# Optimization experiments

Measured on AMD Instinct MI355X. Metric: run time of the kernel, lower is better.

Reference implementation:

```python
import jax, jax.numpy as jnp
import numpy as np

B, S, D, H, HD = 2, 4096, 1024, 16, 64   # batch, seq, hidden, heads, head_dim
BLOCK, W = 64, 8                          # block size, local window in blocks (512 tokens)
ROPE_BASE = 10000.0


def _rope_tables(seq_len, dim, dtype):
    inv_freq = 1.0 / (ROPE_BASE ** (jnp.arange(0, dim, 2, dtype=jnp.float32) / dim))
    t = jnp.arange(seq_len, dtype=jnp.float32)
    freqs = jnp.einsum('i,j->ij', t, inv_freq)          # [S, dim/2]
    emb = jnp.concatenate([freqs, freqs], axis=-1)       # [S, dim]
    return jnp.cos(emb).astype(dtype), jnp.sin(emb).astype(dtype)


def _rotate_half(x):
    x1, x2 = x[..., : x.shape[-1] // 2], x[..., x.shape[-1] // 2:]
    return jnp.concatenate([-x2, x1], axis=-1)


def _apply_rope(q, k, position_ids):
    # q, k: [B, H, S, HD]; position_ids: [B, S]
    cos_t, sin_t = _rope_tables(S, HD, q.dtype)
    cos = cos_t[position_ids][:, None, :, :]             # [B, 1, S, HD]
    sin = sin_t[position_ids][:, None, :, :]
    q_emb = q * cos + _rotate_half(q) * sin
    k_emb = k * cos + _rotate_half(k) * sin
    return q_emb, k_emb


def _block_sparse_attention(q, k, v):
    # Causal block-sparse (sliding window of W blocks), DeepSpeed-style layout.
    # q, k, v: [B, H, S, HD]
    nb = S // BLOCK
    scale = 1.0 / jnp.sqrt(jnp.asarray(HD, q.dtype))
    qb = q.reshape(B, H, nb, BLOCK, HD)
    kb = k.reshape(B, H, nb, BLOCK, HD)
    vb = v.reshape(B, H, nb, BLOCK, HD)
    # block-column indices attended by each block-row: i-W+1 .. i
    idx = jnp.arange(nb)[:, None] - jnp.arange(W - 1, -1, -1)[None, :]   # [nb, W]
    valid = idx >= 0
    idxc = jnp.clip(idx, 0, nb - 1)
    kg = kb[:, :, idxc]                                   # [B, H, nb, W, BLOCK, HD]
    vg = vb[:, :, idxc]
    scores = jnp.einsum('bhnqd,bhnwkd->bhnqwk', qb, kg) * scale  # [B,H,nb,BLOCK,W,BLOCK]
    # absolute positions for causal mask within the window
    qpos = (jnp.arange(nb) * BLOCK)[:, None, None, None] + jnp.arange(BLOCK)[None, :, None, None]  # [nb,BLOCK,1,1]
    kpos = (idxc * BLOCK)[:, None, :, None] + jnp.arange(BLOCK)[None, None, None, :]               # [nb,1,W,BLOCK]
    mask = (kpos <= qpos) & valid[:, None, :, None]       # [nb, BLOCK, W, BLOCK]
    neg = jnp.asarray(-1e9, scores.dtype)
    scores = jnp.where(mask[None, None], scores, neg)
    scores = scores.reshape(B, H, nb, BLOCK, W * BLOCK)
    probs = jax.nn.softmax(scores, axis=-1)
    out = jnp.einsum('bhnqk,bhnkd->bhnqd', probs, vg.reshape(B, H, nb, W * BLOCK, HD))
    return out.reshape(B, H, S, HD)


def setup_inputs() -> dict:
    key = jax.random.key(0)
    ks = jax.random.split(key, 5)
    hidden_states = jax.random.normal(ks[0], (B, S, D), dtype=jnp.float32)
    position_ids = jnp.tile(jnp.arange(S, dtype=jnp.int32)[None, :], (B, 1))
    w_init = lambda k: (jax.random.normal(k, (D, D), dtype=jnp.float32) * 0.02)
    return {
        'hidden_states': hidden_states,
        'position_ids': position_ids,
        'wq': w_init(ks[1]),  # stored [in, out]
        'wk': w_init(ks[2]),
        'wv': w_init(ks[3]),
        'wo': w_init(ks[4]),
    }


def reference(hidden_states, position_ids, wq, wk, wv, wo):
    q = jnp.einsum('bsd,de->bse', hidden_states, wq).reshape(B, S, H, HD).transpose(0, 2, 1, 3)
    k = jnp.einsum('bsd,de->bse', hidden_states, wk).reshape(B, S, H, HD).transpose(0, 2, 1, 3)
    v = jnp.einsum('bsd,de->bse', hidden_states, wv).reshape(B, S, H, HD).transpose(0, 2, 1, 3)
    q, k = _apply_rope(q, k, position_ids)
    attn = _block_sparse_attention(q, k, v)               # [B, H, S, HD]
    attn = attn.transpose(0, 2, 1, 3).reshape(B, S, D)
    return jnp.einsum('bsd,de->bse', attn, wo)
```

## Files before the change

kernel.cpp:

```cpp
#include <hip/hip_runtime.h>
#include <cstdint>
#include <cstddef>

#define B_ 2
#define S_ 4096
#define D_ 1024
#define H_ 16
#define HD_ 64
#define NB_ 64
#define W_ 8
#define M_ (B_*S_)

#define QSCALE 0.18033688011112042f
#define LOG2_10000_OVER_32 0.41524101186092034f

typedef __bf16 bf16_t;
typedef __bf16 bf16x8 __attribute__((ext_vector_type(8)));
typedef float f32x4 __attribute__((ext_vector_type(4)));

#define GLOAD_LDS16(gp, lp) \
  __builtin_amdgcn_global_load_lds((__attribute__((address_space(1))) void*)(gp), \
                                   (__attribute__((address_space(3))) void*)(lp), 16, 0, 0)
#define WAITV(n) asm volatile("s_waitcnt vmcnt(" #n ")" ::: "memory")
#define BAR() do { __builtin_amdgcn_s_barrier(); asm volatile("" ::: "memory"); } while (0)

__global__ __launch_bounds__(256) void prep_kernel(const float* __restrict__ hs,
                                                   bf16_t* __restrict__ hsb,
                                                   const float* __restrict__ w0,
                                                   const float* __restrict__ w1,
                                                   const float* __restrict__ w2,
                                                   const float* __restrict__ w3,
                                                   bf16_t* __restrict__ wT) {
  __shared__ float tile[32][33];
  const int bid = blockIdx.x;
  if (bid < (M_ * D_ / 4) / 256) {
    int i = bid * 256 + threadIdx.x;
    float4 v = ((const float4*)hs)[i];
    union { bf16_t b[4]; uint2 u; } cv;
    cv.b[0] = (bf16_t)v.x; cv.b[1] = (bf16_t)v.y; cv.b[2] = (bf16_t)v.z; cv.b[3] = (bf16_t)v.w;
    ((uint2*)hsb)[i] = cv.u;
  } else {
    const int b2 = bid - (M_ * D_ / 4) / 256;
    const int z = b2 >> 10;
    const int rem = b2 & 1023;
    const int bx = rem & 31, by = rem >> 5;
    const float* w = (z == 0) ? w0 : (z == 1) ? w1 : (z == 2) ? w2 : w3;
    bf16_t* wt = wT + (size_t)z * D_ * D_;
    const int tx = threadIdx.x & 31, ty = threadIdx.x >> 5;
    const int x = bx * 32 + tx;
    const int y0 = by * 32;
    for (int i = ty; i < 32; i += 8)
      tile[i][tx] = w[(size_t)(y0 + i) * D_ + x];
    __syncthreads();
    const int x2 = by * 32 + tx;
    const int y2 = bx * 32;
    for (int i = ty; i < 32; i += 8)
      wt[(size_t)(y2 + i) * D_ + x2] = (bf16_t)tile[tx][i];
  }
}

template<int NBC, int NBUF>
__global__ __launch_bounds__(512, 4) void gemm_bk(const bf16_t* __restrict__ A,
                                                  const bf16_t* __restrict__ Bt,
                                                  void* __restrict__ Cbase,
                                                  bf16_t* __restrict__ vt_out,
                                                  const int* __restrict__ pos_ids) {
  const int bid = blockIdx.x;
  const int sid = (bid & 7) * (NBC * 8) + (bid >> 3);
  const int mb = sid / NBC, nb = sid % NBC;
  const int mbase = mb * 128, nbase = nb * 256;
  const int tid = threadIdx.x;
  const int wid = tid >> 6, lane = tid & 63;
  const int quad = lane >> 4, l16 = lane & 15;
  const int wr = wid >> 2, wc = wid & 3;

  __shared__ bf16_t lds[NBUF * 12288];

  const int srow = wid * 16 + (lane >> 2);
  const int schunk = (lane & 3) ^ ((lane >> 3) & 3);
  const bf16_t* gAb = A  + (size_t)(mbase + srow) * D_ + schunk * 8;
  const bf16_t* gBb = Bt + (size_t)(nbase + srow) * D_ + schunk * 8;
  const int quadx = (quad ^ ((l16 >> 1) & 3)) * 8;

#define STAGE(kt) do { \
    bf16_t* pa_ = lds + ((kt) % NBUF) * 12288 + wid * 512; \
    bf16_t* pb_ = lds + ((kt) % NBUF) * 12288 + 4096 + wid * 512; \
    GLOAD_LDS16(gAb + (kt) * 32, pa_); \
    GLOAD_LDS16(gBb + (kt) * 32, pb_); \
    GLOAD_LDS16(gBb + (size_t)128 * D_ + (kt) * 32, pb_ + 4096); } while (0)

  f32x4 acc[4][4];
#pragma unroll
  for (int m = 0; m < 4; ++m)
#pragma unroll
    for (int n = 0; n < 4; ++n) acc[m][n] = (f32x4){0.f, 0.f, 0.f, 0.f};

#define PHASE(kt, STG, WT) do { \
    const bf16_t* Ab_ = lds + ((kt) % NBUF) * 12288; \
    const bf16_t* Bb_ = Ab_ + 4096; \
    bf16x8 af_[4], bf_[4]; \
    _Pragma("unroll") \
    for (int m = 0; m < 4; ++m) \
      af_[m] = *(const bf16x8*)&Ab_[(wr * 64 + m * 16 + l16) * 32 + quadx]; \
    _Pragma("unroll") \
    for (int n = 0; n < 4; ++n) \
      bf_[n] = *(const bf16x8*)&Bb_[(wc * 64 + n * 16 + l16) * 32 + quadx]; \
    STG; \
    __builtin_amdgcn_s_setprio(1); \
    _Pragma("unroll") \
    for (int m = 0; m < 4; ++m) \
      _Pragma("unroll") \
      for (int n = 0; n < 4; ++n) \
        acc[m][n] = __builtin_amdgcn_mfma_f32_16x16x32_bf16(af_[m], bf_[n], acc[m][n], 0, 0, 0); \
    __builtin_amdgcn_s_setprio(0); \
    WT; \
    BAR(); \
  } while (0)

  if constexpr (NBUF == 3) {
    STAGE(0); STAGE(1);
    WAITV(3);
    BAR();
#pragma unroll 3
    for (int kt = 0; kt < 30; ++kt)
      PHASE(kt, STAGE(kt + 2), WAITV(3));
    PHASE(30, (void)0, WAITV(0));
    PHASE(31, (void)0, (void)0);
  } else {
    STAGE(0);
    WAITV(0);
    BAR();
#pragma unroll 2
    for (int kt = 0; kt < 31; ++kt)
      PHASE(kt, STAGE(kt + 1), WAITV(0));
    PHASE(31, (void)0, (void)0);
  }

  if constexpr (NBC == 12) {
    const int zsl = nb >> 2;
    if (zsl < 2) {
      bf16_t* Cp = (bf16_t*)Cbase + (size_t)zsl * M_ * D_;
      const float qsc = (zsl == 0) ? QSCALE : 1.0f;
      float invf[2];
#pragma unroll
      for (int ni = 0; ni < 2; ++ni)
        invf[ni] = __builtin_exp2f(-(float)(ni * 16 + l16) * LOG2_10000_OVER_32);
      const int colb = (nb & 3) * 256 + wc * 64;
#pragma unroll
      for (int m = 0; m < 4; ++m) {
#pragma unroll
        for (int r = 0; r < 4; ++r) {
          int row = mbase + wr * 64 + m * 16 + quad * 4 + r;
          float fpos = (float)pos_ids[row];
#pragma unroll
          for (int ni = 0; ni < 2; ++ni) {
            float sn, cs;
            __sincosf(fpos * invf[ni], &sn, &cs);
            float x1 = acc[m][ni][r], x2 = acc[m][ni + 2][r];
            int col = colb + ni * 16 + l16;
            Cp[(size_t)row * D_ + col]      = (bf16_t)((x1 * cs - x2 * sn) * qsc);
            Cp[(size_t)row * D_ + col + 32] = (bf16_t)((x2 * cs + x1 * sn) * qsc);
          }
        }
      }
    } else {
      const int h = (nb & 3) * 4 + wc;
      const int g = mb * 2 + wr;
      const int bb = g >> 6, sblk = g & 63;
      size_t vbase = (size_t)(bb * H_ + h) * HD_ * S_;
#pragma unroll
      for (int n = 0; n < 4; ++n) {
        int d = n * 16 + l16;
        union { bf16_t bv[16]; uint4 u[2]; } pk;
#pragma unroll
        for (int r = 0; r < 4; ++r)
#pragma unroll
          for (int mi = 0; mi < 4; ++mi)
            pk.bv[r * 4 + mi] = (bf16_t)acc[mi][n][r];
        size_t addr = vbase + (size_t)d * S_ + (size_t)sblk * 64 + quad * 16;
        *(uint4*)&vt_out[addr]     = pk.u[0];
        *(uint4*)&vt_out[addr + 8] = pk.u[1];
      }
    }
  } else {
    float* Cp = (float*)Cbase;
#pragma unroll
    for (int m = 0; m < 4; ++m)
#pragma unroll
      for (int n = 0; n < 4; ++n)
#pragma unroll
        for (int r = 0; r < 4; ++r) {
          int row = mbase + wr * 64 + m * 16 + quad * 4 + r;
          int col = nbase + wc * 64 + n * 16 + l16;
          Cp[(size_t)row * D_ + col] = acc[m][n][r];
        }
  }
#undef PHASE
#undef STAGE
}

__global__ __launch_bounds__(256) void attn_kernel(const bf16_t* __restrict__ q,
                                                   const bf16_t* __restrict__ k,
                                                   const bf16_t* __restrict__ vt,
                                                   bf16_t* __restrict__ o) {
  const int m = blockIdx.x, h = blockIdx.y, b = blockIdx.z;
  const int n0 = m * 2, n1 = n0 + 1;
  const int tid = threadIdx.x;
  const int wid = tid >> 6, lane = tid & 63;
  const int quad = lane >> 4, l16 = lane & 15;

  __shared__ bf16_t Ks[2][64 * 64];
  __shared__ bf16_t Vs[2][64 * 64];
  __shared__ bf16_t Ps[4][16 * 72];

  const size_t hoff = (size_t)h * HD_;
  const size_t vtbase = (size_t)(b * H_ + h) * HD_ * S_;
  const size_t rowb[2] = {(size_t)(b * S_ + n0 * 64), (size_t)(b * S_ + n1 * 64)};

  bf16x8 aq[2][2];
#pragma unroll
  for (int x = 0; x < 2; ++x) {
    const bf16_t* qr = q + (rowb[x] + wid * 16 + l16) * D_ + hoff;
    aq[x][0] = *(const bf16x8*)(qr + quad * 8);
    aq[x][1] = *(const bf16x8*)(qr + 32 + quad * 8);
  }

  f32x4 o_acc[2][4];
  float lsum[2][4];
#pragma unroll
  for (int x = 0; x < 2; ++x)
#pragma unroll
    for (int t = 0; t < 4; ++t) {
      o_acc[x][t] = (f32x4){0.f, 0.f, 0.f, 0.f};
      lsum[x][t] = 0.f;
    }

  const int srK = wid * 16 + (lane >> 3);
  const int scC = ((lane & 7) ^ ((lane >> 3) & 7)) * 8;
  const bf16_t* kbase = k + (size_t)(b * S_) * D_ + hoff;
  const bf16_t* vbase2 = vt + vtbase;
#define STAGE_KV(kb_, buf_) do { \
    bf16_t* kd = &Ks[buf_][wid * 1024]; \
    bf16_t* vd = &Vs[buf_][wid * 1024]; \
    GLOAD_LDS16(kbase + (size_t)((kb_) * 64 + srK) * D_ + scC, kd); \
    GLOAD_LDS16(kbase + (size_t)((kb_) * 64 + srK + 8) * D_ + scC, kd + 512); \
    GLOAD_LDS16(vbase2 + (size_t)srK * S_ + (kb_) * 64 + scC, vd); \
    GLOAD_LDS16(vbase2 + (size_t)(srK + 8) * S_ + (kb_) * 64 + scC, vd + 512); \
  } while (0)

  const int ck0 = (quad ^ (l16 & 7)) * 8;
  const int ck1 = ((quad ^ 4) ^ (l16 & 7)) * 8;

  const int kb0 = (n0 >= W_ - 1) ? n0 - (W_ - 1) : 0;

  STAGE_KV(kb0, kb0 & 1);

  for (int kb = kb0; kb <= n1; ++kb) {
    const int buf = kb & 1;
    if (kb < n1) { STAGE_KV(kb + 1, buf ^ 1); WAITV(4); }
    else        { WAITV(0); }
    BAR();

#pragma unroll
    for (int x = 0; x < 2; ++x) {
      const int nx = n0 + x;
      if (x == 0 ? (kb > n0) : (kb < n1 - (W_ - 1))) continue;

      f32x4 sacc[4];
#pragma unroll
      for (int t = 0; t < 4; ++t) sacc[t] = (f32x4){0.f, 0.f, 0.f, 0.f};
#pragma unroll
      for (int t = 0; t < 4; ++t) {
        const int rr = (t * 16 + l16) * 64;
        bf16x8 bk0 = *(const bf16x8*)&Ks[buf][rr + ck0];
        bf16x8 bk1 = *(const bf16x8*)&Ks[buf][rr + ck1];
        sacc[t] = __builtin_amdgcn_mfma_f32_16x16x32_bf16(aq[x][0], bk0, sacc[t], 0, 0, 0);
        sacc[t] = __builtin_amdgcn_mfma_f32_16x16x32_bf16(aq[x][1], bk1, sacc[t], 0, 0, 0);
      }

      const bool diag = (kb == nx);
#pragma unroll
      for (int r = 0; r < 4; ++r) {
        int qpos = wid * 16 + quad * 4 + r;
        union { bf16_t bv[4]; uint2 u; } pk;
        float rs = 0.f;
#pragma unroll
        for (int t = 0; t < 4; ++t) {
          float p = __builtin_exp2f(sacc[t][r]);
          if (diag && (t * 16 + l16 > qpos)) p = 0.f;
          rs += p;
          pk.bv[t] = (bf16_t)p;
        }
        lsum[x][r] += rs;
        *(uint2*)&Ps[wid][(quad * 4 + r) * 72 + l16 * 4] = pk.u;
      }

      bf16x8 pa0 = *(const bf16x8*)&Ps[wid][l16 * 72 + quad * 8];
      bf16x8 pa1 = *(const bf16x8*)&Ps[wid][l16 * 72 + 32 + quad * 8];
#pragma unroll
      for (int t = 0; t < 4; ++t) {
        const int rr = (t * 16 + l16) * 64;
        bf16x8 vb0 = *(const bf16x8*)&Vs[buf][rr + ck0];
        bf16x8 vb1 = *(const bf16x8*)&Vs[buf][rr + ck1];
        o_acc[x][t] = __builtin_amdgcn_mfma_f32_16x16x32_bf16(pa0, vb0, o_acc[x][t], 0, 0, 0);
        o_acc[x][t] = __builtin_amdgcn_mfma_f32_16x16x32_bf16(pa1, vb1, o_acc[x][t], 0, 0, 0);
      }
    }
    BAR();
  }
#undef STAGE_KV

#pragma unroll
  for (int x = 0; x < 2; ++x) {
    float inv[4];
#pragma unroll
    for (int r = 0; r < 4; ++r) {
      float s = lsum[x][r];
#pragma unroll
      for (int off = 1; off < 16; off <<= 1) s += __shfl_xor(s, off);
      inv[r] = 1.f / s;
    }
#pragma unroll
    for (int t = 0; t < 4; ++t)
#pragma unroll
      for (int r = 0; r < 4; ++r) {
        int row = wid * 16 + quad * 4 + r;
        int col = t * 16 + l16;
        o[(rowb[x] + row) * D_ + hoff + col] = (bf16_t)(o_acc[x][t][r] * inv[r]);
      }
  }
}

extern "C" void kernel_launch(void* const* d_in, const int* in_sizes, int n_in,
                              void* d_out, int out_size, void* d_ws, size_t ws_size,
                              hipStream_t stream) {
  const float* hs = (const float*)d_in[0];
  const int* pos  = (const int*)d_in[1];
  const float* wq = (const float*)d_in[2];
  const float* wk = (const float*)d_in[3];
  const float* wv = (const float*)d_in[4];
  const float* wo = (const float*)d_in[5];

  bf16_t* ws   = (bf16_t*)d_ws;
  bf16_t* hsb  = ws;
  bf16_t* wT   = hsb + (size_t)M_ * D_;
  bf16_t* qkv  = wT + (size_t)4 * D_ * D_;
  bf16_t* attn = qkv + (size_t)3 * M_ * D_;
  bf16_t* qw  = qkv;
  bf16_t* kw  = qkv + (size_t)M_ * D_;
  bf16_t* vtg = qkv + (size_t)2 * M_ * D_;

  prep_kernel<<<dim3((M_ * D_ / 4) / 256 + 4 * 1024), 256, 0, stream>>>(hs, hsb, wq, wk, wv, wo, wT);
  gemm_bk<12, 2><<<dim3(768), dim3(512), 0, stream>>>(hsb, wT, (void*)qkv, vtg, pos);
  attn_kernel<<<dim3(NB_ / 2, H_, B_), 256, 0, stream>>>(qw, kw, vtg, attn);
  gemm_bk<4, 3><<<dim3(256), dim3(512), 0, stream>>>(attn, wT + (size_t)3 * D_ * D_, d_out, nullptr, pos);
}
```

Baseline: 230.5 us.

## Split attention query blocks across 8 waves and triple-buffer QKV GEMM

The attention kernel now launches 512 threads per block. Each group of four waves owns one of the two query blocks, where before each wave looped over both. K/V staging is spread over eight waves, so each issues half the loads. Separately, the QKV projection GEMM switches from double to triple buffering, and the now-unused double-buffer path is removed. The aim is more latency hiding and parallelism, at the cost of higher LDS use and possibly lower occupancy for the GEMM, and idle waves during window-edge iterations in attention.

```diff
diff --git a/kernel.cpp b/kernel.cpp
--- a/kernel.cpp
+++ b/kernel.cpp
@@ -117,24 +117,14 @@
     BAR(); \
   } while (0)
 
-  if constexpr (NBUF == 3) {
-    STAGE(0); STAGE(1);
-    WAITV(3);
-    BAR();
+  STAGE(0); STAGE(1);
+  WAITV(3);
+  BAR();
 #pragma unroll 3
-    for (int kt = 0; kt < 30; ++kt)
-      PHASE(kt, STAGE(kt + 2), WAITV(3));
-    PHASE(30, (void)0, WAITV(0));
-    PHASE(31, (void)0, (void)0);
-  } else {
-    STAGE(0);
-    WAITV(0);
-    BAR();
-#pragma unroll 2
-    for (int kt = 0; kt < 31; ++kt)
-      PHASE(kt, STAGE(kt + 1), WAITV(0));
-    PHASE(31, (void)0, (void)0);
-  }
+  for (int kt = 0; kt < 30; ++kt)
+    PHASE(kt, STAGE(kt + 2), WAITV(3));
+  PHASE(30, (void)0, WAITV(0));
+  PHASE(31, (void)0, (void)0);
 
   if constexpr (NBC == 12) {
     const int zsl = nb >> 2;
@@ -199,7 +189,7 @@
 #undef STAGE
 }
 
-__global__ __launch_bounds__(256) void attn_kernel(const bf16_t* __restrict__ q,
+__global__ __launch_bounds__(512) void attn_kernel(const bf16_t* __restrict__ q,
                                                    const bf16_t* __restrict__ k,
                                                    const bf16_t* __restrict__ vt,
                                                    bf16_t* __restrict__ o) {
@@ -208,44 +198,40 @@
   const int tid = threadIdx.x;
   const int wid = tid >> 6, lane = tid & 63;
   const int quad = lane >> 4, l16 = lane & 15;
+  const int xg = wid >> 2;
+  const int wq4 = wid & 3;
+  const int nx = n0 + xg;
 
   __shared__ bf16_t Ks[2][64 * 64];
   __shared__ bf16_t Vs[2][64 * 64];
-  __shared__ bf16_t Ps[4][16 * 72];
+  __shared__ bf16_t Ps[8][16 * 72];
 
   const size_t hoff = (size_t)h * HD_;
   const size_t vtbase = (size_t)(b * H_ + h) * HD_ * S_;
-  const size_t rowb[2] = {(size_t)(b * S_ + n0 * 64), (size_t)(b * S_ + n1 * 64)};
-
-  bf16x8 aq[2][2];
-#pragma unroll
-  for (int x = 0; x < 2; ++x) {
-    const bf16_t* qr = q + (rowb[x] + wid * 16 + l16) * D_ + hoff;
-    aq[x][0] = *(const bf16x8*)(qr + quad * 8);
-    aq[x][1] = *(const bf16x8*)(qr + 32 + quad * 8);
-  }
-
-  f32x4 o_acc[2][4];
-  float lsum[2][4];
-#pragma unroll
-  for (int x = 0; x < 2; ++x)
-#pragma unroll
-    for (int t = 0; t < 4; ++t) {
-      o_acc[x][t] = (f32x4){0.f, 0.f, 0.f, 0.f};
-      lsum[x][t] = 0.f;
-    }
-
-  const int srK = wid * 16 + (lane >> 3);
+  const size_t rowb = (size_t)(b * S_ + nx * 64);
+
+  bf16x8 aq0, aq1;
+  {
+    const bf16_t* qr = q + (rowb + wq4 * 16 + l16) * D_ + hoff;
+    aq0 = *(const bf16x8*)(qr + quad * 8);
+    aq1 = *(const bf16x8*)(qr + 32 + quad * 8);
+  }
+
+  f32x4 o_acc[4];
+  float lsum[4];
+#pragma unroll
+  for (int t = 0; t < 4; ++t) {
+    o_acc[t] = (f32x4){0.f, 0.f, 0.f, 0.f};
+    lsum[t] = 0.f;
+  }
+
+  const int srK = wid * 8 + (lane >> 3);
   const int scC = ((lane & 7) ^ ((lane >> 3) & 7)) * 8;
   const bf16_t* kbase = k + (size_t)(b * S_) * D_ + hoff;
   const bf16_t* vbase2 = vt + vtbase;
 #define STAGE_KV(kb_, buf_) do { \
-    bf16_t* kd = &Ks[buf_][wid * 1024]; \
-    bf16_t* vd = &Vs[buf_][wid * 1024]; \
-    GLOAD_LDS16(kbase + (size_t)((kb_) * 64 + srK) * D_ + scC, kd); \
-    GLOAD_LDS16(kbase + (size_t)((kb_) * 64 + srK + 8) * D_ + scC, kd + 512); \
-    GLOAD_LDS16(vbase2 + (size_t)srK * S_ + (kb_) * 64 + scC, vd); \
-    GLOAD_LDS16(vbase2 + (size_t)(srK + 8) * S_ + (kb_) * 64 + scC, vd + 512); \
+    GLOAD_LDS16(kbase + (size_t)((kb_) * 64 + srK) * D_ + scC, &Ks[buf_][wid * 512]); \
+    GLOAD_LDS16(vbase2 + (size_t)srK * S_ + (kb_) * 64 + scC, &Vs[buf_][wid * 512]); \
   } while (0)
 
   const int ck0 = (quad ^ (l16 & 7)) * 8;
@@ -257,15 +243,12 @@
 
   for (int kb = kb0; kb <= n1; ++kb) {
     const int buf = kb & 1;
-    if (kb < n1) { STAGE_KV(kb + 1, buf ^ 1); WAITV(4); }
+    if (kb < n1) { STAGE_KV(kb + 1, buf ^ 1); WAITV(2); }
     else        { WAITV(0); }
     BAR();
 
-#pragma unroll
-    for (int x = 0; x < 2; ++x) {
-      const int nx = n0 + x;
-      if (x == 0 ? (kb > n0) : (kb < n1 - (W_ - 1))) continue;
-
+    const bool active = (xg == 0) ? (kb <= n0) : (kb >= n1 - (W_ - 1));
+    if (active) {
       f32x4 sacc[4];
 #pragma unroll
       for (int t = 0; t < 4; ++t) sacc[t] = (f32x4){0.f, 0.f, 0.f, 0.f};
@@ -274,14 +257,14 @@
         const int rr = (t * 16 + l16) * 64;
         bf16x8 bk0 = *(const bf16x8*)&Ks[buf][rr + ck0];
         bf16x8 bk1 = *(const bf16x8*)&Ks[buf][rr + ck1];
-        sacc[t] = __builtin_amdgcn_mfma_f32_16x16x32_bf16(aq[x][0], bk0, sacc[t], 0, 0, 0);
-        sacc[t] = __builtin_amdgcn_mfma_f32_16x16x32_bf16(aq[x][1], bk1, sacc[t], 0, 0, 0);
+        sacc[t] = __builtin_amdgcn_mfma_f32_16x16x32_bf16(aq0, bk0, sacc[t], 0, 0, 0);
+        sacc[t] = __builtin_amdgcn_mfma_f32_16x16x32_bf16(aq1, bk1, sacc[t], 0, 0, 0);
       }
 
       const bool diag = (kb == nx);
 #pragma unroll
       for (int r = 0; r < 4; ++r) {
-        int qpos = wid * 16 + quad * 4 + r;
+        int qpos = wq4 * 16 + quad * 4 + r;
         union { bf16_t bv[4]; uint2 u; } pk;
         float rs = 0.f;
 #pragma unroll
@@ -291,7 +274,7 @@
           rs += p;
           pk.bv[t] = (bf16_t)p;
         }
-        lsum[x][r] += rs;
+        lsum[r] += rs;
         *(uint2*)&Ps[wid][(quad * 4 + r) * 72 + l16 * 4] = pk.u;
       }
 
@@ -302,33 +285,30 @@
         const int rr = (t * 16 + l16) * 64;
         bf16x8 vb0 = *(const bf16x8*)&Vs[buf][rr + ck0];
         bf16x8 vb1 = *(const bf16x8*)&Vs[buf][rr + ck1];
-        o_acc[x][t] = __builtin_amdgcn_mfma_f32_16x16x32_bf16(pa0, vb0, o_acc[x][t], 0, 0, 0);
-        o_acc[x][t] = __builtin_amdgcn_mfma_f32_16x16x32_bf16(pa1, vb1, o_acc[x][t], 0, 0, 0);
+        o_acc[t] = __builtin_amdgcn_mfma_f32_16x16x32_bf16(pa0, vb0, o_acc[t], 0, 0, 0);
+        o_acc[t] = __builtin_amdgcn_mfma_f32_16x16x32_bf16(pa1, vb1, o_acc[t], 0, 0, 0);
       }
     }
     BAR();
   }
 #undef STAGE_KV
 
-#pragma unroll
-  for (int x = 0; x < 2; ++x) {
-    float inv[4];
+  float inv[4];
+#pragma unroll
+  for (int r = 0; r < 4; ++r) {
+    float s = lsum[r];
+#pragma unroll
+    for (int off = 1; off < 16; off <<= 1) s += __shfl_xor(s, off);
+    inv[r] = 1.f / s;
+  }
+#pragma unroll
+  for (int t = 0; t < 4; ++t)
 #pragma unroll
     for (int r = 0; r < 4; ++r) {
-      float s = lsum[x][r];
-#pragma unroll
-      for (int off = 1; off < 16; off <<= 1) s += __shfl_xor(s, off);
-      inv[r] = 1.f / s;
+      int row = wq4 * 16 + quad * 4 + r;
+      int col = t * 16 + l16;
+      o[(rowb + row) * D_ + hoff + col] = (bf16_t)(o_acc[t][r] * inv[r]);
     }
-#pragma unroll
-    for (int t = 0; t < 4; ++t)
-#pragma unroll
-      for (int r = 0; r < 4; ++r) {
-        int row = wid * 16 + quad * 4 + r;
-        int col = t * 16 + l16;
-        o[(rowb[x] + row) * D_ + hoff + col] = (bf16_t)(o_acc[x][t][r] * inv[r]);
-      }
-  }
 }
 
 extern "C" void kernel_launch(void* const* d_in, const int* in_sizes, int n_in,
@@ -351,7 +331,7 @@
   bf16_t* vtg = qkv + (size_t)2 * M_ * D_;
 
   prep_kernel<<<dim3((M_ * D_ / 4) / 256 + 4 * 1024), 256, 0, stream>>>(hs, hsb, wq, wk, wv, wo, wT);
-  gemm_bk<12, 2><<<dim3(768), dim3(512), 0, stream>>>(hsb, wT, (void*)qkv, vtg, pos);
-  attn_kernel<<<dim3(NB_ / 2, H_, B_), 256, 0, stream>>>(qw, kw, vtg, attn);
+  gemm_bk<12, 3><<<dim3(768), dim3(512), 0, stream>>>(hsb, wT, (void*)qkv, vtg, pos);
+  attn_kernel<<<dim3(NB_ / 2, H_, B_), 512, 0, stream>>>(qw, kw, vtg, attn);
   gemm_bk<4, 3><<<dim3(256), dim3(512), 0, stream>>>(attn, wT + (size_t)3 * D_ * D_, d_out, nullptr, pos);
 }
```

Result: faster. 219.4 us (-4.8%).
